# Kernel tuning notes

Measured on AMD Instinct MI355X. Metric: run time of the kernel, lower is better.

## Reference

```python
import jax, jax.numpy as jnp
import numpy as np

N_NODES = 50000
N_EDGES = 800000
N_NODE_DICT = 10000
N_EDGE_DICT = 100
EMB = 128
HID = 32
HEADS = 4
SLOPE = 0.2
LN_EPS = 1e-5


def layer_norm(x, gamma, beta):
    mu = jnp.mean(x, axis=-1, keepdims=True)
    var = jnp.mean(jnp.square(x - mu), axis=-1, keepdims=True)
    return (x - mu) * jax.lax.rsqrt(var + LN_EPS) * gamma + beta


def setup_inputs() -> dict:
    key = jax.random.key(0)
    ks = jax.random.split(key, 10)
    D = HID * HEADS
    inp = {
        "node_features": jax.random.randint(ks[0], (N_NODES,), 0, N_NODE_DICT),
        "edge_features": jax.random.randint(ks[1], (N_EDGES,), 0, N_EDGE_DICT),
        "edge_index": jax.random.randint(ks[2], (2, N_EDGES), 0, N_NODES),
        "node_emb": jax.random.normal(ks[3], (N_NODE_DICT, EMB), jnp.float32),
        "edge_emb": jax.random.normal(ks[4], (N_EDGE_DICT, EMB), jnp.float32),
        "w_W": jax.random.normal(ks[5], (EMB, D), jnp.float32) / np.sqrt(EMB),
        "w_b": jnp.zeros((D,), jnp.float32),
        "ew_W": jax.random.normal(ks[6], (EMB, D), jnp.float32) / np.sqrt(EMB),
        "ew_b": jnp.zeros((D,), jnp.float32),
        "attn": jax.random.normal(ks[7], (HEADS, 3 * HID), jnp.float32) * 0.1,
        "ln_gamma": jnp.ones((D,), jnp.float32),
        "ln_beta": jnp.zeros((D,), jnp.float32),
    }
    return inp


def reference(node_features, edge_features, edge_index, node_emb, edge_emb,
              w_W, w_b, ew_W, ew_b, attn, ln_gamma, ln_beta):
    # embedding lookups
    nf = node_emb[node_features]                       # [N, EMB]
    ef = edge_emb[edge_features]                       # [E, EMB]
    # linear projections -> [*, heads, hid]
    h = (nf @ w_W + w_b).reshape(-1, HEADS, HID)       # [N, H, F]
    eh = (ef @ ew_W + ew_b).reshape(-1, HEADS, HID)    # [E, H, F]
    tgt = edge_index[0]
    src = edge_index[1]
    # attn = [a_i || a_j || a_e]; dot with concat == sum of per-part dots
    a_i, a_j, a_e = attn[:, :HID], attn[:, HID:2 * HID], attn[:, 2 * HID:]
    s_i = jnp.einsum('nhf,hf->nh', h, a_i)             # [N, H]
    s_j = jnp.einsum('nhf,hf->nh', h, a_j)             # [N, H]
    s_e = jnp.einsum('ehf,hf->eh', eh, a_e)            # [E, H]
    eij = jax.nn.leaky_relu(s_i[tgt] + s_j[src] + s_e, negative_slope=SLOPE)  # [E, H]
    # scatter softmax over edges grouped by target node
    m = jax.ops.segment_max(eij, tgt, num_segments=N_NODES)   # [N, H]
    ex = jnp.exp(eij - m[tgt])
    denom = jax.ops.segment_sum(ex, tgt, num_segments=N_NODES)
    alpha = ex / denom[tgt]                            # [E, H]
    # message passing + scatter_add
    message = alpha[..., None] * h[src]                # [E, H, F]
    out = jax.ops.segment_sum(message, tgt, num_segments=N_NODES)  # [N, H, F]
    out = out + h                                      # skip connection
    out = out.reshape(-1, HEADS * HID)                 # concat heads
    eh2 = eh.reshape(-1, HEADS * HID)
    out = layer_norm(out, ln_gamma, ln_beta)
    eh2 = layer_norm(eh2, ln_gamma, ln_beta)
    return out, eh2
```

## Files before the change

### kernel.cpp

```cpp
#include <hip/hip_runtime.h>

#define NNODES 50000
#define NEDGES 800000
#define NNODE_DICT 10000
#define NEDGE_DICT 100
#define EMB 128
#define HID 32
#define HEADS 4
#define DD 128
#define SLOPE 0.2f
#define LN_EPS 1e-5f
#define NEG_BIG -3.0e38f

typedef float vfloat4 __attribute__((ext_vector_type(4)));

__global__ void node_dict_kernel(const float* __restrict__ node_emb,
                                 const float* __restrict__ w_W,
                                 const float* __restrict__ w_b,
                                 const float* __restrict__ attn,
                                 float* __restrict__ h_dict,
                                 float* __restrict__ s_i_d,
                                 float* __restrict__ s_j_d) {
    __shared__ float a_row[EMB];
    int row = blockIdx.x;
    int col = threadIdx.x;
    a_row[col] = node_emb[row * EMB + col];
    __syncthreads();
    float acc = 0.f;
    #pragma unroll 8
    for (int k = 0; k < EMB; ++k) acc += a_row[k] * w_W[k * DD + col];
    acc += w_b[col];
    h_dict[row * DD + col] = acc;

    int head = col >> 5, f = col & 31;
    float pi = acc * attn[head * 96 + f];
    float pj = acc * attn[head * 96 + 32 + f];
    #pragma unroll
    for (int off = 16; off > 0; off >>= 1) {
        pi += __shfl_down(pi, off);
        pj += __shfl_down(pj, off);
    }
    if ((col & 31) == 0) {
        s_i_d[row * HEADS + head] = pi;
        s_j_d[row * HEADS + head] = pj;
    }
}

__global__ void edge_dict_kernel(const float* __restrict__ edge_emb,
                                 const float* __restrict__ ew_W,
                                 const float* __restrict__ ew_b,
                                 const float* __restrict__ attn,
                                 const float* __restrict__ gamma,
                                 const float* __restrict__ beta,
                                 float* __restrict__ eh2_dict,
                                 float* __restrict__ s_e_d) {
    __shared__ float a_row[EMB];
    __shared__ float red[4];
    int row = blockIdx.x;
    int col = threadIdx.x;
    a_row[col] = edge_emb[row * EMB + col];
    __syncthreads();
    float acc = 0.f;
    #pragma unroll 8
    for (int k = 0; k < EMB; ++k) acc += a_row[k] * ew_W[k * DD + col];
    acc += ew_b[col];

    int head = col >> 5, f = col & 31;
    float pe = acc * attn[head * 96 + 64 + f];
    #pragma unroll
    for (int off = 16; off > 0; off >>= 1) pe += __shfl_down(pe, off);
    if ((col & 31) == 0) s_e_d[row * HEADS + head] = pe;

    float s = acc, s2 = acc * acc;
    #pragma unroll
    for (int off = 32; off > 0; off >>= 1) {
        s  += __shfl_down(s, off);
        s2 += __shfl_down(s2, off);
    }
    int wid = col >> 6;
    if ((col & 63) == 0) { red[wid * 2] = s; red[wid * 2 + 1] = s2; }
    __syncthreads();
    s = red[0] + red[2];
    s2 = red[1] + red[3];
    float mu = s * (1.f / DD);
    float var = s2 * (1.f / DD) - mu * mu;
    float r = rsqrtf(var + LN_EPS);
    eh2_dict[row * DD + col] = (acc - mu) * r * gamma[col] + beta[col];
}

__global__ void count_kernel(const int* __restrict__ edge_index,
                             int* __restrict__ counts) {
    int e = blockIdx.x * blockDim.x + threadIdx.x;
    if (e < NEDGES) atomicAdd(&counts[edge_index[e]], 1);
}

__global__ __launch_bounds__(1024) void scan_kernel(const int* __restrict__ counts,
                                                    int* __restrict__ offsets,
                                                    int* __restrict__ cursor) {
    __shared__ int wsum[16], wexcl[16];
    __shared__ int chunktot;
    int tid = threadIdx.x;
    int lane = tid & 63, wid = tid >> 6;
    int carry = 0;
    for (int base = 0; base < NNODES; base += 1024) {
        int i = base + tid;
        int v = (i < NNODES) ? counts[i] : 0;
        int incl = v;
        #pragma unroll
        for (int o = 1; o < 64; o <<= 1) {
            int t = __shfl_up(incl, o);
            if (lane >= o) incl += t;
        }
        if (lane == 63) wsum[wid] = incl;
        __syncthreads();
        if (tid < 16) {
            int w = wsum[tid];
            int iw = w;
            #pragma unroll
            for (int o = 1; o < 16; o <<= 1) {
                int t = __shfl_up(iw, o);
                if (tid >= o) iw += t;
            }
            wexcl[tid] = iw - w;
            if (tid == 15) chunktot = iw;
        }
        __syncthreads();
        int ex = carry + wexcl[wid] + incl - v;
        if (i < NNODES) { offsets[i] = ex; cursor[i] = ex; }
        carry += chunktot;
        __syncthreads();
    }
    if (tid == 0) offsets[NNODES] = carry;
}

__global__ void scatter_kernel(const int* __restrict__ edge_index,
                               const int* __restrict__ node_features,
                               const int* __restrict__ edge_features,
                               const float4* __restrict__ s_i_d,
                               const float4* __restrict__ s_j_d,
                               const float4* __restrict__ s_e_d,
                               int* __restrict__ cursor,
                               float4* __restrict__ csr_eij,
                               int* __restrict__ csr_ns) {
    int e = blockIdx.x * blockDim.x + threadIdx.x;
    if (e >= NEDGES) return;
    int tgt = edge_index[e];
    int src = edge_index[NEDGES + e];
    int nt = node_features[tgt];
    int ns = node_features[src];
    int ee = edge_features[e];
    float4 si = s_i_d[nt];
    float4 sj = s_j_d[ns];
    float4 se = s_e_d[ee];
    float4 v;
    v.x = si.x + sj.x + se.x; v.x = v.x > 0.f ? v.x : SLOPE * v.x;
    v.y = si.y + sj.y + se.y; v.y = v.y > 0.f ? v.y : SLOPE * v.y;
    v.z = si.z + sj.z + se.z; v.z = v.z > 0.f ? v.z : SLOPE * v.z;
    v.w = si.w + sj.w + se.w; v.w = v.w > 0.f ? v.w : SLOPE * v.w;
    int pos = atomicAdd(&cursor[tgt], 1);
    csr_eij[pos] = v;
    csr_ns[pos] = ns;
}

__global__ __launch_bounds__(128) void node_agg_kernel(
        const int* __restrict__ offsets,
        const float4* __restrict__ csr_eij,
        const int* __restrict__ csr_ns,
        const int* __restrict__ node_features,
        const float* __restrict__ h_dict,
        const float* __restrict__ gamma,
        const float* __restrict__ beta,
        float* __restrict__ out) {
    __shared__ float4 red4[2];
    __shared__ float al[128 * 4];
    __shared__ int nsl[128];
    __shared__ float redln[4];
    int n = blockIdx.x;
    int tid = threadIdx.x;
    int h = tid >> 5;
    int off = offsets[n];
    int deg = offsets[n + 1] - off;

    float4 mrun = make_float4(NEG_BIG, NEG_BIG, NEG_BIG, NEG_BIG);
    float4 lrun = make_float4(0.f, 0.f, 0.f, 0.f);
    float acc = 0.f;

    for (int base = 0; base < deg; base += 128) {
        int cnt = min(deg - base, 128);
        float4 ev = make_float4(NEG_BIG, NEG_BIG, NEG_BIG, NEG_BIG);
        int ns = 0;
        if (tid < cnt) {
            ev = csr_eij[off + base + tid];
            ns = csr_ns[off + base + tid];
        }
        float4 mv = ev;
        #pragma unroll
        for (int o = 32; o > 0; o >>= 1) {
            mv.x = fmaxf(mv.x, __shfl_xor(mv.x, o));
            mv.y = fmaxf(mv.y, __shfl_xor(mv.y, o));
            mv.z = fmaxf(mv.z, __shfl_xor(mv.z, o));
            mv.w = fmaxf(mv.w, __shfl_xor(mv.w, o));
        }
        if ((tid & 63) == 0) red4[tid >> 6] = mv;
        __syncthreads();
        float4 cm;
        cm.x = fmaxf(red4[0].x, red4[1].x);
        cm.y = fmaxf(red4[0].y, red4[1].y);
        cm.z = fmaxf(red4[0].z, red4[1].z);
        cm.w = fmaxf(red4[0].w, red4[1].w);
        float4 newm;
        newm.x = fmaxf(mrun.x, cm.x);
        newm.y = fmaxf(mrun.y, cm.y);
        newm.z = fmaxf(mrun.z, cm.z);
        newm.w = fmaxf(mrun.w, cm.w);
        float4 p = make_float4(0.f, 0.f, 0.f, 0.f);
        if (tid < cnt) {
            p.x = __expf(ev.x - newm.x);
            p.y = __expf(ev.y - newm.y);
            p.z = __expf(ev.z - newm.z);
            p.w = __expf(ev.w - newm.w);
        }
        float4 sv = p;
        #pragma unroll
        for (int o = 32; o > 0; o >>= 1) {
            sv.x += __shfl_xor(sv.x, o);
            sv.y += __shfl_xor(sv.y, o);
            sv.z += __shfl_xor(sv.z, o);
            sv.w += __shfl_xor(sv.w, o);
        }
        __syncthreads();
        if ((tid & 63) == 0) red4[tid >> 6] = sv;
        if (tid < cnt) {
            al[tid * 4 + 0] = p.x; al[tid * 4 + 1] = p.y;
            al[tid * 4 + 2] = p.z; al[tid * 4 + 3] = p.w;
            nsl[tid] = ns;
        }
        __syncthreads();
        float4 cl;
        cl.x = red4[0].x + red4[1].x;
        cl.y = red4[0].y + red4[1].y;
        cl.z = red4[0].z + red4[1].z;
        cl.w = red4[0].w + red4[1].w;
        float4 scale;
        scale.x = __expf(mrun.x - newm.x);
        scale.y = __expf(mrun.y - newm.y);
        scale.z = __expf(mrun.z - newm.z);
        scale.w = __expf(mrun.w - newm.w);
        lrun.x = lrun.x * scale.x + cl.x;
        lrun.y = lrun.y * scale.y + cl.y;
        lrun.z = lrun.z * scale.z + cl.z;
        lrun.w = lrun.w * scale.w + cl.w;
        mrun = newm;
        acc *= (h == 0 ? scale.x : h == 1 ? scale.y : h == 2 ? scale.z : scale.w);
        for (int t = 0; t < cnt; ++t)
            acc += al[t * 4 + h] * h_dict[nsl[t] * DD + tid];
        __syncthreads();
    }

    float lh = (h == 0 ? lrun.x : h == 1 ? lrun.y : h == 2 ? lrun.z : lrun.w);
    float msg = lh > 0.f ? acc / lh : 0.f;
    float v = msg + h_dict[node_features[n] * DD + tid];
    float s = v, s2 = v * v;
    #pragma unroll
    for (int o = 32; o > 0; o >>= 1) {
        s  += __shfl_xor(s, o);
        s2 += __shfl_xor(s2, o);
    }
    if ((tid & 63) == 0) { redln[(tid >> 6) * 2] = s; redln[(tid >> 6) * 2 + 1] = s2; }
    __syncthreads();
    s = redln[0] + redln[2];
    s2 = redln[1] + redln[3];
    float mu = s * (1.f / DD);
    float var = s2 * (1.f / DD) - mu * mu;
    float r = rsqrtf(var + LN_EPS);
    out[n * DD + tid] = (v - mu) * r * gamma[tid] + beta[tid];
}

__global__ void edge_out_kernel(const int* __restrict__ edge_features,
                                const vfloat4* __restrict__ eh2_dict4,
                                vfloat4* __restrict__ out4) {
    int t = blockIdx.x * blockDim.x + threadIdx.x;
    int e = t >> 5;
    int j = t & 31;
    if (e >= NEDGES) return;
    int ee = edge_features[e];
    vfloat4 v = eh2_dict4[ee * 32 + j];
    __builtin_nontemporal_store(v, out4 + (size_t)t);
}

extern "C" void kernel_launch(void* const* d_in, const int* in_sizes, int n_in,
                              void* d_out, int out_size, void* d_ws, size_t ws_size,
                              hipStream_t stream) {
    const int*   node_features = (const int*)d_in[0];
    const int*   edge_features = (const int*)d_in[1];
    const int*   edge_index    = (const int*)d_in[2];
    const float* node_emb      = (const float*)d_in[3];
    const float* edge_emb      = (const float*)d_in[4];
    const float* w_W           = (const float*)d_in[5];
    const float* w_b           = (const float*)d_in[6];
    const float* ew_W          = (const float*)d_in[7];
    const float* ew_b          = (const float*)d_in[8];
    const float* attn          = (const float*)d_in[9];
    const float* gamma         = (const float*)d_in[10];
    const float* beta          = (const float*)d_in[11];

    float* out_nodes = (float*)d_out;
    float* out_edges = (float*)d_out + (size_t)NNODES * DD;

    char* w = (char*)d_ws;
    float*  h_dict   = (float*)w;  w += (size_t)NNODE_DICT * DD * 4;
    float*  s_i_d    = (float*)w;  w += (size_t)NNODE_DICT * 4 * 4;
    float*  s_j_d    = (float*)w;  w += (size_t)NNODE_DICT * 4 * 4;
    float*  eh2_dict = (float*)w;  w += (size_t)NEDGE_DICT * DD * 4;
    float*  s_e_d    = (float*)w;  w += (size_t)NEDGE_DICT * 4 * 4;
    int*    counts   = (int*)w;    w += (size_t)NNODES * 4;
    int*    offsets  = (int*)w;    w += (size_t)(NNODES + 4) * 4;
    int*    cursor   = (int*)w;    w += (size_t)NNODES * 4;
    float4* csr_eij  = (float4*)w; w += (size_t)NEDGES * 16;
    int*    csr_ns   = (int*)w;    w += (size_t)NEDGES * 4;

    (void)hipMemsetAsync(counts, 0, (size_t)NNODES * 4, stream);

    node_dict_kernel<<<NNODE_DICT, 128, 0, stream>>>(node_emb, w_W, w_b, attn,
                                                     h_dict, s_i_d, s_j_d);
    edge_dict_kernel<<<NEDGE_DICT, 128, 0, stream>>>(edge_emb, ew_W, ew_b, attn,
                                                     gamma, beta, eh2_dict, s_e_d);
    count_kernel<<<(NEDGES + 255) / 256, 256, 0, stream>>>(edge_index, counts);
    scan_kernel<<<1, 1024, 0, stream>>>(counts, offsets, cursor);
    scatter_kernel<<<(NEDGES + 255) / 256, 256, 0, stream>>>(edge_index, node_features,
                                                             edge_features,
                                                             (const float4*)s_i_d,
                                                             (const float4*)s_j_d,
                                                             (const float4*)s_e_d,
                                                             cursor, csr_eij, csr_ns);
    node_agg_kernel<<<NNODES, 128, 0, stream>>>(offsets, csr_eij, csr_ns,
                                                node_features, h_dict,
                                                gamma, beta, out_nodes);
    edge_out_kernel<<<(NEDGES * 32 + 255) / 256, 256, 0, stream>>>(edge_features,
                                                                   (const vfloat4*)eh2_dict,
                                                                   (vfloat4*)out_edges);
}
```

Before: 684.5 us.

## Parallelize scan, shrink CSR payload, and use one wavefront per node in aggregation

Several changes land together. The node dictionary projection now handles four rows per block so each weight load is reused, and the edge count reads int4. The single-block scan is replaced by a tiled three-kernel scan. The scatter writes only (src node feature, edge feature) pairs, and the attention logits are computed inside the aggregation kernel. That kernel now assigns one 64-lane wavefront per node with four nodes per block, which removes block-level syncthreads and cuts CSR traffic. The trade-offs are extra launches and a per-edge gather of the attention scores inside aggregation.

```diff
diff --git a/kernel.cpp b/kernel.cpp
--- a/kernel.cpp
+++ b/kernel.cpp
@@ -14,35 +14,53 @@
 
 typedef float vfloat4 __attribute__((ext_vector_type(4)));
 
-__global__ void node_dict_kernel(const float* __restrict__ node_emb,
-                                 const float* __restrict__ w_W,
-                                 const float* __restrict__ w_b,
-                                 const float* __restrict__ attn,
-                                 float* __restrict__ h_dict,
-                                 float* __restrict__ s_i_d,
-                                 float* __restrict__ s_j_d) {
-    __shared__ float a_row[EMB];
-    int row = blockIdx.x;
+__global__ __launch_bounds__(128) void node_dict_kernel(
+        const float* __restrict__ node_emb,
+        const float* __restrict__ w_W,
+        const float* __restrict__ w_b,
+        const float* __restrict__ attn,
+        float* __restrict__ h_dict,
+        float* __restrict__ s_i_d,
+        float* __restrict__ s_j_d) {
+    __shared__ float a_rows[4][EMB];
+    int r0 = blockIdx.x * 4;
     int col = threadIdx.x;
-    a_row[col] = node_emb[row * EMB + col];
+    #pragma unroll
+    for (int r = 0; r < 4; ++r) a_rows[r][col] = node_emb[(r0 + r) * EMB + col];
     __syncthreads();
-    float acc = 0.f;
+    float acc0 = 0.f, acc1 = 0.f, acc2 = 0.f, acc3 = 0.f;
     #pragma unroll 8
-    for (int k = 0; k < EMB; ++k) acc += a_row[k] * w_W[k * DD + col];
-    acc += w_b[col];
-    h_dict[row * DD + col] = acc;
+    for (int k = 0; k < EMB; ++k) {
+        float wv = w_W[k * DD + col];
+        acc0 += a_rows[0][k] * wv;
+        acc1 += a_rows[1][k] * wv;
+        acc2 += a_rows[2][k] * wv;
+        acc3 += a_rows[3][k] * wv;
+    }
+    float b = w_b[col];
+    acc0 += b; acc1 += b; acc2 += b; acc3 += b;
+    h_dict[(r0 + 0) * DD + col] = acc0;
+    h_dict[(r0 + 1) * DD + col] = acc1;
+    h_dict[(r0 + 2) * DD + col] = acc2;
+    h_dict[(r0 + 3) * DD + col] = acc3;
 
     int head = col >> 5, f = col & 31;
-    float pi = acc * attn[head * 96 + f];
-    float pj = acc * attn[head * 96 + 32 + f];
-    #pragma unroll
-    for (int off = 16; off > 0; off >>= 1) {
-        pi += __shfl_down(pi, off);
-        pj += __shfl_down(pj, off);
-    }
-    if ((col & 31) == 0) {
-        s_i_d[row * HEADS + head] = pi;
-        s_j_d[row * HEADS + head] = pj;
+    float ai = attn[head * 96 + f];
+    float aj = attn[head * 96 + 32 + f];
+    float accs[4] = {acc0, acc1, acc2, acc3};
+    #pragma unroll
+    for (int r = 0; r < 4; ++r) {
+        float pi = accs[r] * ai;
+        float pj = accs[r] * aj;
+        #pragma unroll
+        for (int off = 16; off > 0; off >>= 1) {
+            pi += __shfl_down(pi, off);
+            pj += __shfl_down(pj, off);
+        }
+        if ((col & 31) == 0) {
+            s_i_d[(r0 + r) * HEADS + head] = pi;
+            s_j_d[(r0 + r) * HEADS + head] = pj;
+        }
     }
 }
 
@@ -90,108 +108,138 @@
 
 __global__ void count_kernel(const int* __restrict__ edge_index,
                              int* __restrict__ counts) {
-    int e = blockIdx.x * blockDim.x + threadIdx.x;
-    if (e < NEDGES) atomicAdd(&counts[edge_index[e]], 1);
-}
-
-__global__ __launch_bounds__(1024) void scan_kernel(const int* __restrict__ counts,
-                                                    int* __restrict__ offsets,
-                                                    int* __restrict__ cursor) {
-    __shared__ int wsum[16], wexcl[16];
-    __shared__ int chunktot;
+    int i = blockIdx.x * blockDim.x + threadIdx.x;
+    if (i >= NEDGES / 4) return;
+    int4 t = ((const int4*)edge_index)[i];
+    atomicAdd(&counts[t.x], 1);
+    atomicAdd(&counts[t.y], 1);
+    atomicAdd(&counts[t.z], 1);
+    atomicAdd(&counts[t.w], 1);
+}
+
+__global__ __launch_bounds__(256) void scan_tiles(const int* __restrict__ counts,
+                                                  int* __restrict__ excl,
+                                                  int* __restrict__ tsums) {
+    __shared__ int wred[4];
+    int tile = blockIdx.x;
     int tid = threadIdx.x;
-    int lane = tid & 63, wid = tid >> 6;
-    int carry = 0;
-    for (int base = 0; base < NNODES; base += 1024) {
-        int i = base + tid;
-        int v = (i < NNODES) ? counts[i] : 0;
-        int incl = v;
-        #pragma unroll
-        for (int o = 1; o < 64; o <<= 1) {
-            int t = __shfl_up(incl, o);
-            if (lane >= o) incl += t;
-        }
-        if (lane == 63) wsum[wid] = incl;
-        __syncthreads();
-        if (tid < 16) {
-            int w = wsum[tid];
-            int iw = w;
-            #pragma unroll
-            for (int o = 1; o < 16; o <<= 1) {
-                int t = __shfl_up(iw, o);
-                if (tid >= o) iw += t;
-            }
-            wexcl[tid] = iw - w;
-            if (tid == 15) chunktot = iw;
-        }
-        __syncthreads();
-        int ex = carry + wexcl[wid] + incl - v;
-        if (i < NNODES) { offsets[i] = ex; cursor[i] = ex; }
-        carry += chunktot;
-        __syncthreads();
-    }
-    if (tid == 0) offsets[NNODES] = carry;
+    int base = tile * 1024 + tid * 4;
+    int4 v = make_int4(0, 0, 0, 0);
+    if (base + 3 < NNODES) {
+        v = *(const int4*)(counts + base);
+    } else {
+        if (base + 0 < NNODES) v.x = counts[base + 0];
+        if (base + 1 < NNODES) v.y = counts[base + 1];
+        if (base + 2 < NNODES) v.z = counts[base + 2];
+        if (base + 3 < NNODES) v.w = counts[base + 3];
+    }
+    int tsum = v.x + v.y + v.z + v.w;
+    int lane = tid & 63, w = tid >> 6;
+    int incl = tsum;
+    #pragma unroll
+    for (int o = 1; o < 64; o <<= 1) {
+        int t = __shfl_up(incl, o);
+        if (lane >= o) incl += t;
+    }
+    if (lane == 63) wred[w] = incl;
+    __syncthreads();
+    int wexc = 0;
+    #pragma unroll
+    for (int j = 0; j < 4; ++j) if (j < w) wexc += wred[j];
+    int ex = wexc + incl - tsum;
+    int4 o4 = make_int4(ex, ex + v.x, ex + v.x + v.y, ex + v.x + v.y + v.z);
+    if (base + 3 < NNODES) {
+        *(int4*)(excl + base) = o4;
+    } else {
+        if (base + 0 < NNODES) excl[base + 0] = o4.x;
+        if (base + 1 < NNODES) excl[base + 1] = o4.y;
+        if (base + 2 < NNODES) excl[base + 2] = o4.z;
+        if (base + 3 < NNODES) excl[base + 3] = o4.w;
+    }
+    if (tid == 255) tsums[tile] = wexc + incl;
+}
+
+__global__ void scan_sums(int* __restrict__ tsums, int ntiles,
+                          int* __restrict__ total) {
+    int lane = threadIdx.x;
+    int v = (lane < ntiles) ? tsums[lane] : 0;
+    int incl = v;
+    #pragma unroll
+    for (int o = 1; o < 64; o <<= 1) {
+        int t = __shfl_up(incl, o);
+        if (lane >= o) incl += t;
+    }
+    if (lane < ntiles) tsums[lane] = incl - v;
+    if (lane == 63) *total = incl;
+}
+
+__global__ void scan_fixup(const int* __restrict__ tsums,
+                           int* __restrict__ offsets,
+                           int* __restrict__ cursor) {
+    int i = blockIdx.x * blockDim.x + threadIdx.x;
+    if (i >= NNODES) return;
+    int v = offsets[i] + tsums[i >> 10];
+    offsets[i] = v;
+    cursor[i] = v;
 }
 
 __global__ void scatter_kernel(const int* __restrict__ edge_index,
                                const int* __restrict__ node_features,
                                const int* __restrict__ edge_features,
-                               const float4* __restrict__ s_i_d,
-                               const float4* __restrict__ s_j_d,
-                               const float4* __restrict__ s_e_d,
                                int* __restrict__ cursor,
-                               float4* __restrict__ csr_eij,
-                               int* __restrict__ csr_ns) {
+                               int2* __restrict__ csr) {
     int e = blockIdx.x * blockDim.x + threadIdx.x;
     if (e >= NEDGES) return;
     int tgt = edge_index[e];
     int src = edge_index[NEDGES + e];
-    int nt = node_features[tgt];
     int ns = node_features[src];
     int ee = edge_features[e];
-    float4 si = s_i_d[nt];
-    float4 sj = s_j_d[ns];
-    float4 se = s_e_d[ee];
-    float4 v;
-    v.x = si.x + sj.x + se.x; v.x = v.x > 0.f ? v.x : SLOPE * v.x;
-    v.y = si.y + sj.y + se.y; v.y = v.y > 0.f ? v.y : SLOPE * v.y;
-    v.z = si.z + sj.z + se.z; v.z = v.z > 0.f ? v.z : SLOPE * v.z;
-    v.w = si.w + sj.w + se.w; v.w = v.w > 0.f ? v.w : SLOPE * v.w;
     int pos = atomicAdd(&cursor[tgt], 1);
-    csr_eij[pos] = v;
-    csr_ns[pos] = ns;
-}
-
-__global__ __launch_bounds__(128) void node_agg_kernel(
+    csr[pos] = make_int2(ns, ee);
+}
+
+__global__ __launch_bounds__(256) void node_agg_kernel(
         const int* __restrict__ offsets,
-        const float4* __restrict__ csr_eij,
-        const int* __restrict__ csr_ns,
+        const int2* __restrict__ csr,
         const int* __restrict__ node_features,
+        const float4* __restrict__ s_i4,
+        const float4* __restrict__ s_j4,
+        const float4* __restrict__ s_e4,
         const float* __restrict__ h_dict,
         const float* __restrict__ gamma,
         const float* __restrict__ beta,
         float* __restrict__ out) {
-    __shared__ float4 red4[2];
-    __shared__ float al[128 * 4];
-    __shared__ int nsl[128];
-    __shared__ float redln[4];
-    int n = blockIdx.x;
-    int tid = threadIdx.x;
-    int h = tid >> 5;
+    __shared__ float sp[4][256];
+    __shared__ int   sns[4][64];
+    int wid = threadIdx.x >> 6;
+    int lane = threadIdx.x & 63;
+    int n = blockIdx.x * 4 + wid;
+    if (n >= NNODES) return;
+
+    int nt = node_features[n];
+    float4 si = s_i4[nt];
     int off = offsets[n];
     int deg = offsets[n + 1] - off;
 
-    float4 mrun = make_float4(NEG_BIG, NEG_BIG, NEG_BIG, NEG_BIG);
-    float4 lrun = make_float4(0.f, 0.f, 0.f, 0.f);
-    float acc = 0.f;
-
-    for (int base = 0; base < deg; base += 128) {
-        int cnt = min(deg - base, 128);
+    float m0 = NEG_BIG, m1 = NEG_BIG, m2 = NEG_BIG, m3 = NEG_BIG;
+    float l0 = 0.f, l1 = 0.f, l2 = 0.f, l3 = 0.f;
+    float acc0 = 0.f, acc1 = 0.f;
+    int h0 = lane >> 5;
+    int h1 = 2 + (lane >> 5);
+
+    for (int base = 0; base < deg; base += 64) {
+        int cnt = min(deg - base, 64);
         float4 ev = make_float4(NEG_BIG, NEG_BIG, NEG_BIG, NEG_BIG);
         int ns = 0;
-        if (tid < cnt) {
-            ev = csr_eij[off + base + tid];
-            ns = csr_ns[off + base + tid];
+        if (lane < cnt) {
+            int2 pr = csr[off + base + lane];
+            ns = pr.x;
+            float4 sj = s_j4[pr.x];
+            float4 se = s_e4[pr.y];
+            ev.x = si.x + sj.x + se.x; ev.x = ev.x > 0.f ? ev.x : SLOPE * ev.x;
+            ev.y = si.y + sj.y + se.y; ev.y = ev.y > 0.f ? ev.y : SLOPE * ev.y;
+            ev.z = si.z + sj.z + se.z; ev.z = ev.z > 0.f ? ev.z : SLOPE * ev.z;
+            ev.w = si.w + sj.w + se.w; ev.w = ev.w > 0.f ? ev.w : SLOPE * ev.w;
         }
         float4 mv = ev;
         #pragma unroll
@@ -201,24 +249,14 @@
             mv.z = fmaxf(mv.z, __shfl_xor(mv.z, o));
             mv.w = fmaxf(mv.w, __shfl_xor(mv.w, o));
         }
-        if ((tid & 63) == 0) red4[tid >> 6] = mv;
-        __syncthreads();
-        float4 cm;
-        cm.x = fmaxf(red4[0].x, red4[1].x);
-        cm.y = fmaxf(red4[0].y, red4[1].y);
-        cm.z = fmaxf(red4[0].z, red4[1].z);
-        cm.w = fmaxf(red4[0].w, red4[1].w);
-        float4 newm;
-        newm.x = fmaxf(mrun.x, cm.x);
-        newm.y = fmaxf(mrun.y, cm.y);
-        newm.z = fmaxf(mrun.z, cm.z);
-        newm.w = fmaxf(mrun.w, cm.w);
+        float nm0 = fmaxf(m0, mv.x), nm1 = fmaxf(m1, mv.y);
+        float nm2 = fmaxf(m2, mv.z), nm3 = fmaxf(m3, mv.w);
         float4 p = make_float4(0.f, 0.f, 0.f, 0.f);
-        if (tid < cnt) {
-            p.x = __expf(ev.x - newm.x);
-            p.y = __expf(ev.y - newm.y);
-            p.z = __expf(ev.z - newm.z);
-            p.w = __expf(ev.w - newm.w);
+        if (lane < cnt) {
+            p.x = __expf(ev.x - nm0);
+            p.y = __expf(ev.y - nm1);
+            p.z = __expf(ev.z - nm2);
+            p.w = __expf(ev.w - nm3);
         }
         float4 sv = p;
         #pragma unroll
@@ -228,52 +266,49 @@
             sv.z += __shfl_xor(sv.z, o);
             sv.w += __shfl_xor(sv.w, o);
         }
-        __syncthreads();
-        if ((tid & 63) == 0) red4[tid >> 6] = sv;
-        if (tid < cnt) {
-            al[tid * 4 + 0] = p.x; al[tid * 4 + 1] = p.y;
-            al[tid * 4 + 2] = p.z; al[tid * 4 + 3] = p.w;
-            nsl[tid] = ns;
-        }
-        __syncthreads();
-        float4 cl;
-        cl.x = red4[0].x + red4[1].x;
-        cl.y = red4[0].y + red4[1].y;
-        cl.z = red4[0].z + red4[1].z;
-        cl.w = red4[0].w + red4[1].w;
-        float4 scale;
-        scale.x = __expf(mrun.x - newm.x);
-        scale.y = __expf(mrun.y - newm.y);
-        scale.z = __expf(mrun.z - newm.z);
-        scale.w = __expf(mrun.w - newm.w);
-        lrun.x = lrun.x * scale.x + cl.x;
-        lrun.y = lrun.y * scale.y + cl.y;
-        lrun.z = lrun.z * scale.z + cl.z;
-        lrun.w = lrun.w * scale.w + cl.w;
-        mrun = newm;
-        acc *= (h == 0 ? scale.x : h == 1 ? scale.y : h == 2 ? scale.z : scale.w);
-        for (int t = 0; t < cnt; ++t)
-            acc += al[t * 4 + h] * h_dict[nsl[t] * DD + tid];
-        __syncthreads();
-    }
-
-    float lh = (h == 0 ? lrun.x : h == 1 ? lrun.y : h == 2 ? lrun.z : lrun.w);
-    float msg = lh > 0.f ? acc / lh : 0.f;
-    float v = msg + h_dict[node_features[n] * DD + tid];
-    float s = v, s2 = v * v;
+        float sc0 = __expf(m0 - nm0), sc1 = __expf(m1 - nm1);
+        float sc2 = __expf(m2 - nm2), sc3 = __expf(m3 - nm3);
+        l0 = l0 * sc0 + sv.x; l1 = l1 * sc1 + sv.y;
+        l2 = l2 * sc2 + sv.z; l3 = l3 * sc3 + sv.w;
+        m0 = nm0; m1 = nm1; m2 = nm2; m3 = nm3;
+        acc0 *= (lane < 32) ? sc0 : sc1;
+        acc1 *= (lane < 32) ? sc2 : sc3;
+        if (lane < cnt) {
+            sp[wid][lane * 4 + 0] = p.x;
+            sp[wid][lane * 4 + 1] = p.y;
+            sp[wid][lane * 4 + 2] = p.z;
+            sp[wid][lane * 4 + 3] = p.w;
+            sns[wid][lane] = ns;
+        }
+        int nst = sns[wid][0];
+        for (int t = 0; t < cnt; ++t) {
+            const float* hr = h_dict + (size_t)nst * DD;
+            float w0 = sp[wid][t * 4 + h0];
+            float w1 = sp[wid][t * 4 + h1];
+            if (t + 1 < cnt) nst = sns[wid][t + 1];
+            acc0 += w0 * hr[lane];
+            acc1 += w1 * hr[lane + 64];
+        }
+    }
+
+    float den0 = (lane < 32) ? l0 : l1;
+    float den1 = (lane < 32) ? l2 : l3;
+    float msg0 = den0 > 0.f ? acc0 / den0 : 0.f;
+    float msg1 = den1 > 0.f ? acc1 / den1 : 0.f;
+    const float* hres = h_dict + (size_t)nt * DD;
+    float v0 = msg0 + hres[lane];
+    float v1 = msg1 + hres[lane + 64];
+    float s = v0 + v1, s2 = v0 * v0 + v1 * v1;
     #pragma unroll
     for (int o = 32; o > 0; o >>= 1) {
         s  += __shfl_xor(s, o);
         s2 += __shfl_xor(s2, o);
     }
-    if ((tid & 63) == 0) { redln[(tid >> 6) * 2] = s; redln[(tid >> 6) * 2 + 1] = s2; }
-    __syncthreads();
-    s = redln[0] + redln[2];
-    s2 = redln[1] + redln[3];
     float mu = s * (1.f / DD);
     float var = s2 * (1.f / DD) - mu * mu;
     float r = rsqrtf(var + LN_EPS);
-    out[n * DD + tid] = (v - mu) * r * gamma[tid] + beta[tid];
+    out[(size_t)n * DD + lane]      = (v0 - mu) * r * gamma[lane] + beta[lane];
+    out[(size_t)n * DD + lane + 64] = (v1 - mu) * r * gamma[lane + 64] + beta[lane + 64];
 }
 
 __global__ void edge_out_kernel(const int* __restrict__ edge_features,
@@ -308,34 +343,36 @@
     float* out_edges = (float*)d_out + (size_t)NNODES * DD;
 
     char* w = (char*)d_ws;
-    float*  h_dict   = (float*)w;  w += (size_t)NNODE_DICT * DD * 4;
-    float*  s_i_d    = (float*)w;  w += (size_t)NNODE_DICT * 4 * 4;
-    float*  s_j_d    = (float*)w;  w += (size_t)NNODE_DICT * 4 * 4;
-    float*  eh2_dict = (float*)w;  w += (size_t)NEDGE_DICT * DD * 4;
-    float*  s_e_d    = (float*)w;  w += (size_t)NEDGE_DICT * 4 * 4;
-    int*    counts   = (int*)w;    w += (size_t)NNODES * 4;
-    int*    offsets  = (int*)w;    w += (size_t)(NNODES + 4) * 4;
-    int*    cursor   = (int*)w;    w += (size_t)NNODES * 4;
-    float4* csr_eij  = (float4*)w; w += (size_t)NEDGES * 16;
-    int*    csr_ns   = (int*)w;    w += (size_t)NEDGES * 4;
+    float* h_dict   = (float*)w;  w += (size_t)NNODE_DICT * DD * 4;
+    float* s_i_d    = (float*)w;  w += (size_t)NNODE_DICT * 4 * 4;
+    float* s_j_d    = (float*)w;  w += (size_t)NNODE_DICT * 4 * 4;
+    float* eh2_dict = (float*)w;  w += (size_t)NEDGE_DICT * DD * 4;
+    float* s_e_d    = (float*)w;  w += (size_t)NEDGE_DICT * 4 * 4;
+    int*   counts   = (int*)w;    w += (size_t)NNODES * 4;
+    int*   offsets  = (int*)w;    w += (size_t)(NNODES + 4) * 4;
+    int*   cursor   = (int*)w;    w += (size_t)NNODES * 4;
+    int*   tsums    = (int*)w;    w += (size_t)64 * 4;
+    int2*  csr      = (int2*)w;   w += (size_t)NEDGES * 8;
+
+    const int ntiles = (NNODES + 1023) / 1024;
 
     (void)hipMemsetAsync(counts, 0, (size_t)NNODES * 4, stream);
 
-    node_dict_kernel<<<NNODE_DICT, 128, 0, stream>>>(node_emb, w_W, w_b, attn,
-                                                     h_dict, s_i_d, s_j_d);
+    node_dict_kernel<<<NNODE_DICT / 4, 128, 0, stream>>>(node_emb, w_W, w_b, attn,
+                                                         h_dict, s_i_d, s_j_d);
     edge_dict_kernel<<<NEDGE_DICT, 128, 0, stream>>>(edge_emb, ew_W, ew_b, attn,
                                                      gamma, beta, eh2_dict, s_e_d);
-    count_kernel<<<(NEDGES + 255) / 256, 256, 0, stream>>>(edge_index, counts);
-    scan_kernel<<<1, 1024, 0, stream>>>(counts, offsets, cursor);
+    count_kernel<<<(NEDGES / 4 + 255) / 256, 256, 0, stream>>>(edge_index, counts);
+    scan_tiles<<<ntiles, 256, 0, stream>>>(counts, offsets, tsums);
+    scan_sums<<<1, 64, 0, stream>>>(tsums, ntiles, offsets + NNODES);
+    scan_fixup<<<(NNODES + 255) / 256, 256, 0, stream>>>(tsums, offsets, cursor);
     scatter_kernel<<<(NEDGES + 255) / 256, 256, 0, stream>>>(edge_index, node_features,
-                                                             edge_features,
-                                                             (const float4*)s_i_d,
-                                                             (const float4*)s_j_d,
-                                                             (const float4*)s_e_d,
-                                                             cursor, csr_eij, csr_ns);
-    node_agg_kernel<<<NNODES, 128, 0, stream>>>(offsets, csr_eij, csr_ns,
-                                                node_features, h_dict,
-                                                gamma, beta, out_nodes);
+                                                             edge_features, cursor, csr);
+    node_agg_kernel<<<(NNODES + 3) / 4, 256, 0, stream>>>(offsets, csr, node_features,
+                                                          (const float4*)s_i_d,
+                                                          (const float4*)s_j_d,
+                                                          (const float4*)s_e_d,
+                                                          h_dict, gamma, beta, out_nodes);
     edge_out_kernel<<<(NEDGES * 32 + 255) / 256, 256, 0, stream>>>(edge_features,
                                                                    (const vfloat4*)eh2_dict,
                                                                    (vfloat4*)out_edges);
```

New measurement: 600.1 us. 12.3% less time.
